# Kernel tuning notes

Hardware: AMD Instinct MI355X
Metric: run time of the kernel (lower is better)

Reference implementation:

```python
import jax, jax.numpy as jnp
import numpy as np
import math

IN_DIM = 512
LR_MUL = 1.0
SCALE = (1.0 / math.sqrt(IN_DIM)) * LR_MUL  # EqualLinear runtime weight scale


def setup_inputs() -> dict:
    key = jax.random.key(0)
    k1, k2 = jax.random.split(key)
    x = jax.random.normal(k1, (256, 18, 18, 512), dtype=jnp.float32)  # [B, n_out, n_layers, in_dim]
    W = jax.random.normal(k2, (18, 512, 512), dtype=jnp.float32)      # [n_out, out_dim, in_dim]
    b = jnp.zeros((18, 512), dtype=jnp.float32)                        # [n_out, out_dim], bias_init=0
    idx = jnp.arange(18, dtype=jnp.int32)                              # n_indx
    return {"x": x, "W": W, "b": b, "idx": idx}


def reference(x, W, b, idx):
    # Fused equivalent of the nested loops: for each direction i, apply
    # EqualLinear_i to slices x[:, i, j, :] for j in idx, writing results back.
    x_sel = x[:, :, idx, :]                                    # [B, O, J, D_in]
    y = jnp.einsum('koji,odi->kojd', x_sel, W) * SCALE         # [B, O, J, D_out]
    y = y + (b * LR_MUL)[None, :, None, :]
    return x.at[:, :, idx, :].set(y)
```

## Files before the change

### kernel.cpp

```cpp
#include <hip/hip_runtime.h>
#include <hip/hip_bf16.h>


typedef __bf16  bf16x8  __attribute__((ext_vector_type(8)));
typedef float   floatx4 __attribute__((ext_vector_type(4)));

#define O_DIM 18
#define J_DIM 18
#define KB    256
#define C_DIM 512
#define BM    128
#define BN    128
#define BK    32
#define LDSS  40

__device__ __forceinline__ __bf16 f2bf(float f) {
    return (__bf16)f;
}

__global__ __launch_bounds__(256, 2)
void dirnet_gemm(const float* __restrict__ x, const float* __restrict__ W,
                 const float* __restrict__ bias, const int* __restrict__ idx,
                 float* __restrict__ out)
{
    const int nt = blockIdx.x & 3;
    const int mt = blockIdx.x >> 2;
    const int j  = blockIdx.y;
    const int o  = blockIdx.z;
    const int jj = idx[j];

    __shared__ __bf16 As[BM * LDSS];
    __shared__ __bf16 Bs[BN * LDSS];

    const int tid  = threadIdx.x;
    const int srow = tid >> 2;
    const int scol = (tid & 3) << 3;

    const size_t xRow0      = ((size_t)((mt * BM + srow) * O_DIM + o) * J_DIM + jj) * C_DIM;
    const size_t xRowStride = (size_t)64 * O_DIM * J_DIM * C_DIM;
    const size_t wRow0      = ((size_t)(o * C_DIM + nt * BN + srow)) * C_DIM;
    const size_t wRowStride = (size_t)64 * C_DIM;

    const int lane = tid & 63;
    const int wv   = tid >> 6;
    const int mOff = (wv & 1) * 64;
    const int nOff = (wv >> 1) * 64;
    const int lrow = lane & 15;
    const int lk   = (lane >> 4) << 3;

    floatx4 acc[4][4] = {};

    for (int k0 = 0; k0 < C_DIM; k0 += BK) {
        __syncthreads();
        #pragma unroll
        for (int p = 0; p < 2; ++p) {
            const float* ap = x + xRow0 + (size_t)p * xRowStride + k0 + scol;
            const float4 ua = *(const float4*)ap;
            const float4 va = *(const float4*)(ap + 4);
            const float* bp = W + wRow0 + (size_t)p * wRowStride + k0 + scol;
            const float4 ub = *(const float4*)bp;
            const float4 vb = *(const float4*)(bp + 4);

            bf16x8 sa;
            sa[0]=f2bf(ua.x); sa[1]=f2bf(ua.y); sa[2]=f2bf(ua.z); sa[3]=f2bf(ua.w);
            sa[4]=f2bf(va.x); sa[5]=f2bf(va.y); sa[6]=f2bf(va.z); sa[7]=f2bf(va.w);
            *(bf16x8*)&As[(p * 64 + srow) * LDSS + scol] = sa;

            bf16x8 sb;
            sb[0]=f2bf(ub.x); sb[1]=f2bf(ub.y); sb[2]=f2bf(ub.z); sb[3]=f2bf(ub.w);
            sb[4]=f2bf(vb.x); sb[5]=f2bf(vb.y); sb[6]=f2bf(vb.z); sb[7]=f2bf(vb.w);
            *(bf16x8*)&Bs[(p * 64 + srow) * LDSS + scol] = sb;
        }
        __syncthreads();

        bf16x8 af[4], bf[4];
        #pragma unroll
        for (int mi = 0; mi < 4; ++mi)
            af[mi] = *(const bf16x8*)&As[(mOff + mi * 16 + lrow) * LDSS + lk];
        #pragma unroll
        for (int ni = 0; ni < 4; ++ni)
            bf[ni] = *(const bf16x8*)&Bs[(nOff + ni * 16 + lrow) * LDSS + lk];

        #pragma unroll
        for (int mi = 0; mi < 4; ++mi)
            #pragma unroll
            for (int ni = 0; ni < 4; ++ni)
                acc[mi][ni] = __builtin_amdgcn_mfma_f32_16x16x32_bf16(
                    af[mi], bf[ni], acc[mi][ni], 0, 0, 0);
    }

    const float scale = 0.04419417382415922f;
    const int rbase = (lane >> 4) << 2;
    #pragma unroll
    for (int ni = 0; ni < 4; ++ni) {
        const int d  = nt * BN + nOff + ni * 16 + lrow;
        const float bv = bias[o * C_DIM + d];
        #pragma unroll
        for (int mi = 0; mi < 4; ++mi) {
            #pragma unroll
            for (int r = 0; r < 4; ++r) {
                const int kr = mt * BM + mOff + mi * 16 + rbase + r;
                out[((size_t)(kr * O_DIM + o) * J_DIM + jj) * C_DIM + d] =
                    acc[mi][ni][r] * scale + bv;
            }
        }
    }
}

__global__ void copy_nonsel(const float* __restrict__ x, const int* __restrict__ idx,
                            float* __restrict__ out)
{
    const int jj = blockIdx.x;
    const int o  = blockIdx.y;
    bool member = false;
    for (int t = 0; t < J_DIM; ++t) member = member || (idx[t] == jj);
    if (member) return;
    const int tid = threadIdx.x;
    for (int k = 0; k < KB; ++k) {
        const size_t base = ((size_t)(k * O_DIM + o) * J_DIM + jj) * C_DIM;
        for (int c = tid * 4; c < C_DIM; c += 256 * 4) {
            *(float4*)&out[base + c] = *(const float4*)&x[base + c];
        }
    }
}

extern "C" void kernel_launch(void* const* d_in, const int* in_sizes, int n_in,
                              void* d_out, int out_size, void* d_ws, size_t ws_size,
                              hipStream_t stream) {
    const float* x   = (const float*)d_in[0];
    const float* W   = (const float*)d_in[1];
    const float* b   = (const float*)d_in[2];
    const int*   idx = (const int*)d_in[3];
    float* out = (float*)d_out;

    dim3 grid(8, J_DIM, O_DIM);
    dirnet_gemm<<<grid, 256, 0, stream>>>(x, W, b, idx, out);
    copy_nonsel<<<dim3(J_DIM, O_DIM), 256, 0, stream>>>(x, idx, out);
}
```

Baseline: 389.5 us.

## Double-buffer LDS with register prefetch, remap blocks per XCD, nontemporal stores

The GEMM main loop now prefetches the next K-slice of x and W into registers while MFMAs run on the current LDS buffer. The LDS tiles are double-buffered, so only one barrier per iteration is needed. The grid is flattened and remapped so that blocks sharing the same (o,j) W/x tiles land on the same XCD. Output stores use nontemporal hints and launch bounds request 3 blocks per CU, which raises register pressure and LDS use per block.

```diff
diff --git a/kernel.cpp b/kernel.cpp
--- a/kernel.cpp
+++ b/kernel.cpp
@@ -12,25 +12,29 @@
 #define BM    128
 #define BN    128
 #define BK    32
+#define NK    (C_DIM / BK)
 #define LDSS  40
 
-__device__ __forceinline__ __bf16 f2bf(float f) {
-    return (__bf16)f;
-}
+__device__ __forceinline__ __bf16 f2bf(float f) { return (__bf16)f; }
 
-__global__ __launch_bounds__(256, 2)
+__global__ __launch_bounds__(256, 3)
 void dirnet_gemm(const float* __restrict__ x, const float* __restrict__ W,
                  const float* __restrict__ bias, const int* __restrict__ idx,
                  float* __restrict__ out)
 {
-    const int nt = blockIdx.x & 3;
-    const int mt = blockIdx.x >> 2;
-    const int j  = blockIdx.y;
-    const int o  = blockIdx.z;
-    const int jj = idx[j];
+    const int id   = blockIdx.x;
+    const int xcd  = id & 7;
+    const int slot = id >> 3;
+    const int nt   = slot & 3;
+    const int g    = (slot >> 2) * 8 + xcd;
+    const int mt   = g & 1;
+    const int jo   = g >> 1;
+    const int j    = jo % J_DIM;
+    const int o    = jo / J_DIM;
+    const int jj   = idx[j];
 
-    __shared__ __bf16 As[BM * LDSS];
-    __shared__ __bf16 Bs[BN * LDSS];
+    __shared__ __bf16 As[2][BM * LDSS];
+    __shared__ __bf16 Bs[2][BM * LDSS];
 
     const int tid  = threadIdx.x;
     const int srow = tid >> 2;
@@ -49,44 +53,67 @@
     const int lk   = (lane >> 4) << 3;
 
     floatx4 acc[4][4] = {};
+    float4 pa[2][2], pb[2][2];
 
-    for (int k0 = 0; k0 < C_DIM; k0 += BK) {
-        __syncthreads();
+    #pragma unroll
+    for (int p = 0; p < 2; ++p) {
+        const float* ap = x + xRow0 + (size_t)p * xRowStride + scol;
+        pa[p][0] = *(const float4*)ap;
+        pa[p][1] = *(const float4*)(ap + 4);
+        const float* bp = W + wRow0 + (size_t)p * wRowStride + scol;
+        pb[p][0] = *(const float4*)bp;
+        pb[p][1] = *(const float4*)(bp + 4);
+    }
+
+    for (int t = 0; t < NK; ++t) {
+        const int cur = t & 1;
+
         #pragma unroll
         for (int p = 0; p < 2; ++p) {
-            const float* ap = x + xRow0 + (size_t)p * xRowStride + k0 + scol;
-            const float4 ua = *(const float4*)ap;
-            const float4 va = *(const float4*)(ap + 4);
-            const float* bp = W + wRow0 + (size_t)p * wRowStride + k0 + scol;
-            const float4 ub = *(const float4*)bp;
-            const float4 vb = *(const float4*)(bp + 4);
-
             bf16x8 sa;
-            sa[0]=f2bf(ua.x); sa[1]=f2bf(ua.y); sa[2]=f2bf(ua.z); sa[3]=f2bf(ua.w);
-            sa[4]=f2bf(va.x); sa[5]=f2bf(va.y); sa[6]=f2bf(va.z); sa[7]=f2bf(va.w);
-            *(bf16x8*)&As[(p * 64 + srow) * LDSS + scol] = sa;
+            sa[0]=f2bf(pa[p][0].x); sa[1]=f2bf(pa[p][0].y);
+            sa[2]=f2bf(pa[p][0].z); sa[3]=f2bf(pa[p][0].w);
+            sa[4]=f2bf(pa[p][1].x); sa[5]=f2bf(pa[p][1].y);
+            sa[6]=f2bf(pa[p][1].z); sa[7]=f2bf(pa[p][1].w);
+            *(bf16x8*)&As[cur][(p * 64 + srow) * LDSS + scol] = sa;
 
             bf16x8 sb;
-            sb[0]=f2bf(ub.x); sb[1]=f2bf(ub.y); sb[2]=f2bf(ub.z); sb[3]=f2bf(ub.w);
-            sb[4]=f2bf(vb.x); sb[5]=f2bf(vb.y); sb[6]=f2bf(vb.z); sb[7]=f2bf(vb.w);
-            *(bf16x8*)&Bs[(p * 64 + srow) * LDSS + scol] = sb;
+            sb[0]=f2bf(pb[p][0].x); sb[1]=f2bf(pb[p][0].y);
+            sb[2]=f2bf(pb[p][0].z); sb[3]=f2bf(pb[p][0].w);
+            sb[4]=f2bf(pb[p][1].x); sb[5]=f2bf(pb[p][1].y);
+            sb[6]=f2bf(pb[p][1].z); sb[7]=f2bf(pb[p][1].w);
+            *(bf16x8*)&Bs[cur][(p * 64 + srow) * LDSS + scol] = sb;
         }
+
         __syncthreads();
 
-        bf16x8 af[4], bf[4];
+        if (t + 1 < NK) {
+            const int k0 = (t + 1) * BK;
+            #pragma unroll
+            for (int p = 0; p < 2; ++p) {
+                const float* ap = x + xRow0 + (size_t)p * xRowStride + k0 + scol;
+                pa[p][0] = *(const float4*)ap;
+                pa[p][1] = *(const float4*)(ap + 4);
+                const float* bp = W + wRow0 + (size_t)p * wRowStride + k0 + scol;
+                pb[p][0] = *(const float4*)bp;
+                pb[p][1] = *(const float4*)(bp + 4);
+            }
+        }
+
+        bf16x8 af[4], bfr[4];
         #pragma unroll
         for (int mi = 0; mi < 4; ++mi)
-            af[mi] = *(const bf16x8*)&As[(mOff + mi * 16 + lrow) * LDSS + lk];
+            af[mi] = *(const bf16x8*)&As[cur][(mOff + mi * 16 + lrow) * LDSS + lk];
         #pragma unroll
         for (int ni = 0; ni < 4; ++ni)
-            bf[ni] = *(const bf16x8*)&Bs[(nOff + ni * 16 + lrow) * LDSS + lk];
+            bfr[ni] = *(const bf16x8*)&Bs[cur][(nOff + ni * 16 + lrow) * LDSS + lk];
 
         #pragma unroll
         for (int mi = 0; mi < 4; ++mi)
             #pragma unroll
             for (int ni = 0; ni < 4; ++ni)
                 acc[mi][ni] = __builtin_amdgcn_mfma_f32_16x16x32_bf16(
-                    af[mi], bf[ni], acc[mi][ni], 0, 0, 0);
+                    af[mi], bfr[ni], acc[mi][ni], 0, 0, 0);
     }
 
     const float scale = 0.04419417382415922f;
@@ -100,8 +127,9 @@
             #pragma unroll
             for (int r = 0; r < 4; ++r) {
                 const int kr = mt * BM + mOff + mi * 16 + rbase + r;
-                out[((size_t)(kr * O_DIM + o) * J_DIM + jj) * C_DIM + d] =
-                    acc[mi][ni][r] * scale + bv;
+                __builtin_nontemporal_store(
+                    acc[mi][ni][r] * scale + bv,
+                    &out[((size_t)(kr * O_DIM + o) * J_DIM + jj) * C_DIM + d]);
             }
         }
     }
@@ -133,7 +161,6 @@
     const int*   idx = (const int*)d_in[3];
     float* out = (float*)d_out;
 
-    dim3 grid(8, J_DIM, O_DIM);
-    dirnet_gemm<<<grid, 256, 0, stream>>>(x, W, b, idx, out);
+    dirnet_gemm<<<dim3(8 * J_DIM * O_DIM), 256, 0, stream>>>(x, W, b, idx, out);
     copy_nonsel<<<dim3(J_DIM, O_DIM), 256, 0, stream>>>(x, idx, out);
 }
```

Result: slower. 423.2 us (+8.6%).

## Shrink GEMM tile, add register prefetch and XCD-aware block mapping

Applied to the files above, without the earlier changes.

Shrinks the N tile from 128 to 64 and uses 512-thread blocks with a 32x32 output per wave, raising occupancy through the launch bounds. Global loads for the next K step are prefetched into registers while MFMAs run on the current LDS tile. A 1D grid is remapped so that all N-tiles sharing the same x rows land on the same XCD, aiming for better L2 reuse of x. In exchange, each wave does less MFMA work per LDS load, and every x tile is now read by 8 blocks instead of 4.

```diff
diff --git a/kernel.cpp b/kernel.cpp
--- a/kernel.cpp
+++ b/kernel.cpp
@@ -3,6 +3,7 @@
 
 
 typedef __bf16  bf16x8  __attribute__((ext_vector_type(8)));
+typedef __bf16  bf16x4  __attribute__((ext_vector_type(4)));
 typedef float   floatx4 __attribute__((ext_vector_type(4)));
 
 #define O_DIM 18
@@ -10,93 +11,98 @@
 #define KB    256
 #define C_DIM 512
 #define BM    128
-#define BN    128
+#define BN    64
 #define BK    32
+#define NK    (C_DIM / BK)
 #define LDSS  40
 
-__device__ __forceinline__ __bf16 f2bf(float f) {
-    return (__bf16)f;
-}
+__device__ __forceinline__ __bf16 f2bf(float f) { return (__bf16)f; }
 
-__global__ __launch_bounds__(256, 2)
+__global__ __launch_bounds__(512, 6)
 void dirnet_gemm(const float* __restrict__ x, const float* __restrict__ W,
                  const float* __restrict__ bias, const int* __restrict__ idx,
                  float* __restrict__ out)
 {
-    const int nt = blockIdx.x & 3;
-    const int mt = blockIdx.x >> 2;
-    const int j  = blockIdx.y;
-    const int o  = blockIdx.z;
-    const int jj = idx[j];
+    const int id   = blockIdx.x;
+    const int xcd  = id & 7;
+    const int slot = id >> 3;
+    const int nt   = slot & 7;
+    const int g    = (slot >> 3) * 8 + xcd;
+    const int mt   = g & 1;
+    const int jo   = g >> 1;
+    const int j    = jo % J_DIM;
+    const int o    = jo / J_DIM;
+    const int jj   = idx[j];
 
     __shared__ __bf16 As[BM * LDSS];
     __shared__ __bf16 Bs[BN * LDSS];
 
     const int tid  = threadIdx.x;
-    const int srow = tid >> 2;
-    const int scol = (tid & 3) << 3;
+    const int arow = tid >> 2;
+    const int acol = (tid & 3) << 3;
+    const int brow = tid >> 3;
+    const int bcol = (tid & 7) << 2;
 
-    const size_t xRow0      = ((size_t)((mt * BM + srow) * O_DIM + o) * J_DIM + jj) * C_DIM;
-    const size_t xRowStride = (size_t)64 * O_DIM * J_DIM * C_DIM;
-    const size_t wRow0      = ((size_t)(o * C_DIM + nt * BN + srow)) * C_DIM;
-    const size_t wRowStride = (size_t)64 * C_DIM;
+    const float* xp = x + ((size_t)((mt * BM + arow) * O_DIM + o) * J_DIM + jj) * C_DIM + acol;
+    const float* wp = W + ((size_t)(o * C_DIM + nt * BN + brow)) * C_DIM + bcol;
 
     const int lane = tid & 63;
     const int wv   = tid >> 6;
-    const int mOff = (wv & 1) * 64;
-    const int nOff = (wv >> 1) * 64;
+    const int mOff = (wv & 3) * 32;
+    const int nOff = (wv >> 2) * 32;
     const int lrow = lane & 15;
     const int lk   = (lane >> 4) << 3;
 
-    floatx4 acc[4][4] = {};
+    floatx4 acc[2][2] = {};
+    float4 pa0, pa1, pb;
 
-    for (int k0 = 0; k0 < C_DIM; k0 += BK) {
+    pa0 = *(const float4*)(xp);
+    pa1 = *(const float4*)(xp + 4);
+    pb  = *(const float4*)(wp);
+
+    for (int t = 0; t < NK; ++t) {
+        bf16x8 sa;
+        sa[0]=f2bf(pa0.x); sa[1]=f2bf(pa0.y); sa[2]=f2bf(pa0.z); sa[3]=f2bf(pa0.w);
+        sa[4]=f2bf(pa1.x); sa[5]=f2bf(pa1.y); sa[6]=f2bf(pa1.z); sa[7]=f2bf(pa1.w);
+        bf16x4 sb;
+        sb[0]=f2bf(pb.x); sb[1]=f2bf(pb.y); sb[2]=f2bf(pb.z); sb[3]=f2bf(pb.w);
+
         __syncthreads();
-        #pragma unroll
-        for (int p = 0; p < 2; ++p) {
-            const float* ap = x + xRow0 + (size_t)p * xRowStride + k0 + scol;
-            const float4 ua = *(const float4*)ap;
-            const float4 va = *(const float4*)(ap + 4);
-            const float* bp = W + wRow0 + (size_t)p * wRowStride + k0 + scol;
-            const float4 ub = *(const float4*)bp;
-            const float4 vb = *(const float4*)(bp + 4);
-
-            bf16x8 sa;
-            sa[0]=f2bf(ua.x); sa[1]=f2bf(ua.y); sa[2]=f2bf(ua.z); sa[3]=f2bf(ua.w);
-            sa[4]=f2bf(va.x); sa[5]=f2bf(va.y); sa[6]=f2bf(va.z); sa[7]=f2bf(va.w);
-            *(bf16x8*)&As[(p * 64 + srow) * LDSS + scol] = sa;
-
-            bf16x8 sb;
-            sb[0]=f2bf(ub.x); sb[1]=f2bf(ub.y); sb[2]=f2bf(ub.z); sb[3]=f2bf(ub.w);
-            sb[4]=f2bf(vb.x); sb[5]=f2bf(vb.y); sb[6]=f2bf(vb.z); sb[7]=f2bf(vb.w);
-            *(bf16x8*)&Bs[(p * 64 + srow) * LDSS + scol] = sb;
-        }
+        *(bf16x8*)&As[arow * LDSS + acol] = sa;
+        *(bf16x4*)&Bs[brow * LDSS + bcol] = sb;
         __syncthreads();
 
-        bf16x8 af[4], bf[4];
+        if (t + 1 < NK) {
+            const int k0 = (t + 1) * BK;
+            pa0 = *(const float4*)(xp + k0);
+            pa1 = *(const float4*)(xp + k0 + 4);
+            pb  = *(const float4*)(wp + k0);
+        }
+
+        bf16x8 af[2], bfr[2];
         #pragma unroll
-        for (int mi = 0; mi < 4; ++mi)
+        for (int mi = 0; mi < 2; ++mi)
             af[mi] = *(const bf16x8*)&As[(mOff + mi * 16 + lrow) * LDSS + lk];
         #pragma unroll
-        for (int ni = 0; ni < 4; ++ni)
-            bf[ni] = *(const bf16x8*)&Bs[(nOff + ni * 16 + lrow) * LDSS + lk];
+        for (int ni = 0; ni < 2; ++ni)
+            bfr[ni] = *(const bf16x8*)&Bs[(nOff + ni * 16 + lrow) * LDSS + lk];
 
         #pragma unroll
-        for (int mi = 0; mi < 4; ++mi)
+        for (int mi = 0; mi < 2; ++mi)
             #pragma unroll
-            for (int ni = 0; ni < 4; ++ni)
+            for (int ni = 0; ni < 2; ++ni)
                 acc[mi][ni] = __builtin_amdgcn_mfma_f32_16x16x32_bf16(
-                    af[mi], bf[ni], acc[mi][ni], 0, 0, 0);
+                    af[mi], bfr[ni], acc[mi][ni], 0, 0, 0);
     }
 
     const float scale = 0.04419417382415922f;
     const int rbase = (lane >> 4) << 2;
     #pragma unroll
-    for (int ni = 0; ni < 4; ++ni) {
+    for (int ni = 0; ni < 2; ++ni) {
         const int d  = nt * BN + nOff + ni * 16 + lrow;
         const float bv = bias[o * C_DIM + d];
         #pragma unroll
-        for (int mi = 0; mi < 4; ++mi) {
+        for (int mi = 0; mi < 2; ++mi) {
             #pragma unroll
             for (int r = 0; r < 4; ++r) {
                 const int kr = mt * BM + mOff + mi * 16 + rbase + r;
@@ -133,7 +139,6 @@
     const int*   idx = (const int*)d_in[3];
     float* out = (float*)d_out;
 
-    dim3 grid(8, J_DIM, O_DIM);
-    dirnet_gemm<<<grid, 256, 0, stream>>>(x, W, b, idx, out);
+    dirnet_gemm<<<dim3(2 * 8 * J_DIM * O_DIM), 512, 0, stream>>>(x, W, b, idx, out);
     copy_nonsel<<<dim3(J_DIM, O_DIM), 256, 0, stream>>>(x, idx, out);
 }
```

New measurement: 407.7 us. 4.7% more time.
